# Kernel optimization log

Hardware: AMD Instinct MI355X
Metric: run time of the kernel (lower is better)

## Reference

```python
import jax, jax.numpy as jnp
import numpy as np

EPS = 1e-5  # torch BatchNorm2d default eps

def _bn_train(x, g, b):
    # BatchNorm2d in training mode: batch statistics over (N, H, W), biased variance
    m = x.mean(axis=(0, 2, 3), keepdims=True)
    v = x.var(axis=(0, 2, 3), keepdims=True)
    return g[None, :, None, None] * (x - m) / jnp.sqrt(v + EPS) + b[None, :, None, None]

def _conv3(x, w, b):
    y = jax.lax.conv_general_dilated(x, w, (1, 1), 'SAME',
                                     dimension_numbers=('NCHW', 'OIHW', 'NCHW'))
    return y + b[None, :, None, None]

def _conv1(x, w, b):
    # 1x1 conv == per-pixel matmul; w: [out, in]
    return jnp.einsum('bchw,oc->bohw', x, w) + b[None, :, None, None]

def _projector(x, w1, b1, g1, be1, w2, b2, g2, be2):
    h = jax.nn.relu(_bn_train(_conv3(x, w1, b1), g1, be1))
    return _bn_train(_conv1(h, w2, b2), g2, be2)

def _cross_teacher_attention(s, teachers, wq, bq, wk, bk, wv, bv):
    B, C, H, W = s.shape
    scale = C ** -0.5
    q = _conv1(s, wq, bq).reshape(B, C, H * W).transpose(0, 2, 1)  # [B, HW, C]
    outs, ws = [], []
    for t in teachers:  # small fixed list of teachers (structural branch)
        k = _conv1(t, wk, bk).reshape(B, C, H * W).transpose(0, 2, 1)
        v = _conv1(t, wv, bv).reshape(B, C, H * W).transpose(0, 2, 1)
        a = jax.nn.softmax(jnp.einsum('bqc,bkc->bqk', q, k) * scale, axis=-1)  # [B, HW, HW]
        outs.append(jnp.einsum('bqk,bkc->bqc', a, v))                          # [B, HW, C]
        ws.append(a.mean(axis=-1))                                             # [B, HW]
    w = jax.nn.softmax(jnp.stack(ws, axis=-1), axis=-1)          # [B, HW, T]
    fused = jnp.einsum('bqt,tbqc->bqc', w, jnp.stack(outs, 0))   # weighted sum over teachers
    fused = fused.reshape(B, H, W, C).transpose(0, 3, 1, 2)      # [B, C, H, W]
    return s + fused

def setup_inputs() -> dict:
    key = jax.random.key(0)
    ks = jax.random.split(key, 16)
    B, C, H, W = 8, 128, 56, 56
    T = 256  # teacher projector output dim
    d = {}
    d['student_mid'] = jax.random.normal(ks[0], (B, C, H, W), jnp.float32)
    d['t1_mid'] = jax.random.normal(ks[1], (B, C, H, W), jnp.float32)
    d['t2_mid'] = jax.random.normal(ks[2], (B, C, H, W), jnp.float32)
    for i, n in enumerate(['q', 'k', 'v']):
        d['w' + n] = jax.random.normal(ks[3 + i], (C, C), jnp.float32) * 0.05
        d['b' + n] = jnp.zeros((C,), jnp.float32)
    for p, off in (('p1', 6), ('p2', 10)):
        d[p + '_w1'] = jax.random.normal(ks[off], (C, C, 3, 3), jnp.float32) * 0.05
        d[p + '_b1'] = jnp.zeros((C,), jnp.float32)
        d[p + '_g1'] = jnp.ones((C,), jnp.float32)
        d[p + '_be1'] = jnp.zeros((C,), jnp.float32)
        d[p + '_w2'] = jax.random.normal(ks[off + 1], (T, C), jnp.float32) * 0.05
        d[p + '_b2'] = jnp.zeros((T,), jnp.float32)
        d[p + '_g2'] = jnp.ones((T,), jnp.float32)
        d[p + '_be2'] = jnp.zeros((T,), jnp.float32)
    return d

def reference(student_mid, t1_mid, t2_mid, wq, bq, wk, bk, wv, bv,
              p1_w1, p1_b1, p1_g1, p1_be1, p1_w2, p1_b2, p1_g2, p1_be2,
              p2_w1, p2_b1, p2_g1, p2_be1, p2_w2, p2_b2, p2_g2, p2_be2):
    # Per-teacher projectors: computed by the torch module but their outputs are
    # never consumed by the attention (s_feat_proj is unused) -> dead code.
    _sp1 = _projector(student_mid, p1_w1, p1_b1, p1_g1, p1_be1, p1_w2, p1_b2, p1_g2, p1_be2)
    _sp2 = _projector(student_mid, p2_w1, p2_b1, p2_g1, p2_be1, p2_w2, p2_b2, p2_g2, p2_be2)
    del _sp1, _sp2
    return _cross_teacher_attention(student_mid, [t1_mid, t2_mid], wq, bq, wk, bk, wv, bv)
```

## Files before the change

kernel.cpp:

```cpp
#include <hip/hip_runtime.h>

#define HW 3136
#define NB 8
#define CD 128
#define QSCALE 0.12751750206f

typedef __attribute__((ext_vector_type(8))) short short8;
typedef __attribute__((ext_vector_type(4))) float floatx4;
typedef __attribute__((ext_vector_type(4))) unsigned short ushort4v;

static __device__ __forceinline__ unsigned short f2b(float f){
  union { float f; unsigned u; } v; v.f = f;
  unsigned r = v.u + 0x7FFFu + ((v.u >> 16) & 1u);
  return (unsigned short)(r >> 16);
}
static __device__ __forceinline__ float b2f(unsigned short h){
  union { unsigned u; float f; } v; v.u = ((unsigned)h) << 16;
  return v.f;
}

__global__ __launch_bounds__(256) void proj_kernel(
    const float* __restrict__ s, const float* __restrict__ t1, const float* __restrict__ t2,
    const float* __restrict__ wq, const float* __restrict__ bq,
    const float* __restrict__ wk, const float* __restrict__ bk,
    const float* __restrict__ wv, const float* __restrict__ bv,
    unsigned short* __restrict__ qkv)
{
  __shared__ __align__(16) unsigned short WL[CD][136];
  __shared__ __align__(16) unsigned short xsT[64][136];
  const int job = blockIdx.z;
  const float* x; const float* w; const float* bias; float scl; int cmajor; size_t dstoff;
  switch(job){
    case 0: x=s;  w=wq; bias=bq; scl=QSCALE; cmajor=0; dstoff=0; break;
    case 1: x=t1; w=wk; bias=bk; scl=1.f;    cmajor=0; dstoff=1; break;
    case 2: x=t1; w=wv; bias=bv; scl=1.f;    cmajor=1; dstoff=2; break;
    case 3: x=t2; w=wk; bias=bk; scl=1.f;    cmajor=0; dstoff=3; break;
    default:x=t2; w=wv; bias=bv; scl=1.f;    cmajor=1; dstoff=4; break;
  }
  const size_t TS = (size_t)NB*HW*CD;
  const int b   = blockIdx.y;
  const int hw0 = blockIdx.x * 64;
  const int tid = threadIdx.x;

  for (int i = 0; i < 16; i++){
    int flat = tid + i*256;
    int o = flat >> 5, cq = (flat & 31)*4;
    floatx4 wv4 = *(const floatx4*)(w + (size_t)o*CD + cq);
    ushort4v pk;
    for (int j=0;j<4;j++) pk[j] = f2b(wv4[j]);
    *(ushort4v*)&WL[o][cq] = pk;
  }
  const float* xb = x + (size_t)b*CD*HW + hw0;
  for (int i = 0; i < 8; i++){
    int flat = (tid + i*256)*4;
    int c = flat >> 6, hh = flat & 63;
    floatx4 xv = *(const floatx4*)(xb + (size_t)c*HW + hh);
    for (int j=0;j<4;j++) xsT[hh+j][c] = f2b(xv[j]);
  }
  __syncthreads();

  const int m = tid & 15, quad = (tid >> 4) & 3, wv_ = tid >> 6;
  short8 af[4];
  for (int dk=0;dk<4;dk++)
    af[dk] = *(const short8*)&xsT[wv_*16 + m][dk*32 + quad*8];
  float bb[8];
  for (int nt=0;nt<8;nt++) bb[nt] = bias[nt*16 + m];

  unsigned short* dstK = qkv + dstoff*TS + ((size_t)b*HW + hw0)*CD;
  unsigned short* dstV = qkv + dstoff*TS + (size_t)b*CD*HW;
  for (int nt=0;nt<8;nt++){
    floatx4 acc = {bb[nt],bb[nt],bb[nt],bb[nt]};
    for (int dk=0;dk<4;dk++){
      short8 bf = *(const short8*)&WL[nt*16 + m][dk*32 + quad*8];
      acc = __builtin_amdgcn_mfma_f32_16x16x32_bf16(af[dk], bf, acc, 0,0,0);
    }
    if (!cmajor){
      for (int r=0;r<4;r++)
        dstK[(size_t)(wv_*16 + quad*4 + r)*CD + nt*16 + m] = f2b(acc[r]*scl);
    } else {
      ushort4v pk;
      for (int r=0;r<4;r++) pk[r] = f2b(acc[r]*scl);
      *(ushort4v*)&dstV[(size_t)(nt*16 + m)*HW + hw0 + wv_*16 + quad*4] = pk;
    }
  }
}

#define KL_E (64*136)
#define VL_E (128*72)
#define PL_E (4*16*72)

__global__ __launch_bounds__(256,3) void attn_kernel(
    const unsigned short* __restrict__ qkv,
    unsigned short* __restrict__ Og)
{
  __shared__ __align__(16) unsigned short smem[KL_E + VL_E + PL_E];
  unsigned short (*Kl)[136] = (unsigned short(*)[136])smem;
  unsigned short (*Vl)[72]  = (unsigned short(*)[72])(smem + KL_E);
  unsigned short (*Pl)[72]  = (unsigned short(*)[72])(smem + KL_E + VL_E);

  const int qt = blockIdx.x;
  const int b  = blockIdx.y;
  const int t  = blockIdx.z;
  const size_t TS = (size_t)NB*HW*CD;
  const unsigned short* Q = qkv + (size_t)b*HW*CD;
  const unsigned short* K = qkv + TS*(size_t)(1 + 2*t) + (size_t)b*HW*CD;
  const unsigned short* V = qkv + TS*(size_t)(2 + 2*t) + (size_t)b*CD*HW;

  const int tid  = threadIdx.x;
  const int wv_  = tid >> 6;
  const int lane = tid & 63;
  const int m    = lane & 15;
  const int quad = lane >> 4;
  const int q0   = qt*64 + wv_*16;

  short8 qf[4];
  {
    const unsigned short* qr = Q + (size_t)(q0+m)*CD + quad*8;
    for (int dk=0;dk<4;dk++) qf[dk] = *(const short8*)(qr + dk*32);
  }
  floatx4 Oc[8];
  for (int i=0;i<8;i++) Oc[i] = (floatx4)0.f;
  float lr[4] = {0.f,0.f,0.f,0.f};

  const unsigned short* kg = K + (size_t)(tid>>4)*CD + (tid&15)*8;
  const unsigned short* vg = V + (size_t)(tid>>3)*HW + (tid&7)*8;
  unsigned short* klds = &Kl[tid>>4][(tid&15)*8];
  unsigned short* vlds = &Vl[tid>>3][(tid&7)*8];

  short8 kpre[4], vpre[4];
  for (int i=0;i<4;i++) kpre[i] = *(const short8*)(kg + (size_t)i*16*CD);
  for (int i=0;i<4;i++) vpre[i] = *(const short8*)(vg + (size_t)i*32*HW);

  for (int kt = 0; kt < HW/64; kt++){
    __syncthreads();
    for (int i=0;i<4;i++) *(short8*)(klds + i*16*136) = kpre[i];
    for (int i=0;i<4;i++) *(short8*)(vlds + i*32*72)  = vpre[i];
    __syncthreads();
    if (kt < HW/64 - 1){
      kg += 64*CD; vg += 64;
      for (int i=0;i<4;i++) kpre[i] = *(const short8*)(kg + (size_t)i*16*CD);
      for (int i=0;i<4;i++) vpre[i] = *(const short8*)(vg + (size_t)i*32*HW);
    }

    floatx4 sc[4];
    for (int nt=0;nt<4;nt++){
      floatx4 acc = (floatx4)0.f;
      for (int dk=0;dk<4;dk++){
        short8 kf = *(const short8*)&Kl[nt*16 + m][dk*32 + quad*8];
        acc = __builtin_amdgcn_mfma_f32_16x16x32_bf16(qf[dk], kf, acc, 0,0,0);
      }
      sc[nt] = acc;
    }
    for (int nt=0;nt<4;nt++){
      for (int r=0;r<4;r++){
        float p = __builtin_amdgcn_exp2f(sc[nt][r]);
        lr[r] += p;
        union { float f; unsigned u; } cv; cv.f = p;
        Pl[wv_*16 + quad*4 + r][nt*16 + m] = (unsigned short)(cv.u >> 16);
      }
    }
    __asm__ volatile("s_waitcnt lgkmcnt(0)" ::: "memory");
    for (int ct=0;ct<8;ct++){
      floatx4 o = Oc[ct];
      for (int kk=0;kk<2;kk++){
        short8 pf = *(const short8*)&Pl[wv_*16 + m][kk*32 + quad*8];
        short8 vf = *(const short8*)&Vl[ct*16 + m][kk*32 + quad*8];
        o = __builtin_amdgcn_mfma_f32_16x16x32_bf16(pf, vf, o, 0,0,0);
      }
      Oc[ct] = o;
    }
  }

  for (int r=0;r<4;r++)
    for (int off=1; off<16; off<<=1)
      lr[r] += __shfl_xor(lr[r], off, 64);
  float inv[4];
  for (int r=0;r<4;r++) inv[r] = 1.f / lr[r];

  __syncthreads();
  float* stg = ((float*)smem) + wv_*(16*132);
  for (int ct=0;ct<8;ct++)
    for (int r=0;r<4;r++)
      stg[(quad*4+r)*132 + ct*16 + m] = Oc[ct][r]*inv[r];
  __syncthreads();
  unsigned short* ob = Og + ((size_t)t*NB + b)*HW*CD + (size_t)q0*CD;
  for (int row=0; row<16; row++){
    float v0 = stg[row*132 + 2*lane];
    float v1 = stg[row*132 + 2*lane + 1];
    unsigned short pk[2] = {f2b(v0), f2b(v1)};
    *(unsigned int*)&ob[(size_t)row*CD + 2*lane] = *(const unsigned int*)pk;
  }
}

__global__ __launch_bounds__(256) void combine_kernel(
    const float* __restrict__ s, const unsigned short* __restrict__ Og,
    float* __restrict__ out)
{
  __shared__ float T[32][129];
  const int b   = blockIdx.y;
  const int hw0 = blockIdx.x * 32;
  const int tid = threadIdx.x;
  const unsigned short* O1 = Og + ((size_t)b*HW + hw0)*CD;
  const unsigned short* O2 = O1 + (size_t)NB*HW*CD;
  for (int i=0;i<2;i++){
    int flat = (tid + i*256)*8;
    int row = flat >> 7, col = flat & 127;
    short8 a  = *(const short8*)(O1 + (size_t)row*CD + col);
    short8 c2 = *(const short8*)(O2 + (size_t)row*CD + col);
    for (int j=0;j<8;j++)
      T[row][col+j] = 0.5f*(b2f((unsigned short)a[j]) + b2f((unsigned short)c2[j]));
  }
  __syncthreads();
  const int c  = tid >> 1;
  const int h0 = (tid & 1)*16;
  const float* sr = s   + ((size_t)b*CD + c)*HW + hw0 + h0;
  float*     orow = out + ((size_t)b*CD + c)*HW + hw0 + h0;
  for (int j0=0;j0<16;j0+=4){
    floatx4 sv = *(const floatx4*)(sr + j0);
    floatx4 ov;
    for (int jj=0;jj<4;jj++) ov[jj] = sv[jj] + T[h0+j0+jj][c];
    *(floatx4*)(orow + j0) = ov;
  }
}

extern "C" void kernel_launch(void* const* d_in, const int* in_sizes, int n_in,
                              void* d_out, int out_size, void* d_ws, size_t ws_size,
                              hipStream_t stream)
{
  const float* s  = (const float*)d_in[0];
  const float* t1 = (const float*)d_in[1];
  const float* t2 = (const float*)d_in[2];
  const float* wq = (const float*)d_in[3];
  const float* bq = (const float*)d_in[4];
  const float* wk = (const float*)d_in[5];
  const float* bk = (const float*)d_in[6];
  const float* wv = (const float*)d_in[7];
  const float* bv = (const float*)d_in[8];
  float* out = (float*)d_out;

  unsigned short* qkv = (unsigned short*)d_ws;
  unsigned short* Og  = qkv + (size_t)5*NB*HW*CD;

  hipLaunchKernelGGL(proj_kernel,    dim3(49,8,5), dim3(256), 0, stream,
                     s,t1,t2,wq,bq,wk,bk,wv,bv,qkv);
  hipLaunchKernelGGL(attn_kernel,    dim3(49,8,2), dim3(256), 0, stream, qkv, Og);
  hipLaunchKernelGGL(combine_kernel, dim3(98,8),   dim3(256), 0, stream, s, Og, out);
}
```

Before: 310.1 us.

## Use 32x32 MFMA with register-resident P in attention and batch-loop projection

The attention kernel moves to 32x32x16 bf16 MFMA with 128-query tiles per block. It computes S transposed so the exponentiated scores stay in registers and are swapped between half-waves with a shuffle, instead of passing through an LDS P buffer. LDS strides and occupancy bounds also change, and the final normalization and store are restaged. The projection kernel now loops over the batch inside each block, double-buffering the transposed input and reusing the loaded weight tile, which cuts the grid from 1960 to 245 blocks. The risks are lower occupancy and parallelism in proj, padded last query tiles, and possible bank conflicts from the new LDS strides.

Result: slower. 568.2 us (+83.2%).

```diff
diff --git a/kernel.cpp b/kernel.cpp
--- a/kernel.cpp
+++ b/kernel.cpp
@@ -7,6 +7,7 @@
 
 typedef __attribute__((ext_vector_type(8))) short short8;
 typedef __attribute__((ext_vector_type(4))) float floatx4;
+typedef __attribute__((ext_vector_type(16))) float floatx16;
 typedef __attribute__((ext_vector_type(4))) unsigned short ushort4v;
 
 static __device__ __forceinline__ unsigned short f2b(float f){
@@ -14,12 +15,16 @@
   unsigned r = v.u + 0x7FFFu + ((v.u >> 16) & 1u);
   return (unsigned short)(r >> 16);
 }
+static __device__ __forceinline__ unsigned short f2b_trunc(float f){
+  union { float f; unsigned u; } v; v.f = f;
+  return (unsigned short)(v.u >> 16);
+}
 static __device__ __forceinline__ float b2f(unsigned short h){
   union { unsigned u; float f; } v; v.u = ((unsigned)h) << 16;
   return v.f;
 }
 
-__global__ __launch_bounds__(256) void proj_kernel(
+__global__ __launch_bounds__(256,2) void proj_kernel(
     const float* __restrict__ s, const float* __restrict__ t1, const float* __restrict__ t2,
     const float* __restrict__ wq, const float* __restrict__ bq,
     const float* __restrict__ wk, const float* __restrict__ bk,
@@ -27,8 +32,8 @@
     unsigned short* __restrict__ qkv)
 {
   __shared__ __align__(16) unsigned short WL[CD][136];
-  __shared__ __align__(16) unsigned short xsT[64][136];
-  const int job = blockIdx.z;
+  __shared__ __align__(16) unsigned short XT[2][64][136];
+  const int job = blockIdx.y;
   const float* x; const float* w; const float* bias; float scl; int cmajor; size_t dstoff;
   switch(job){
     case 0: x=s;  w=wq; bias=bq; scl=QSCALE; cmajor=0; dstoff=0; break;
@@ -38,7 +43,6 @@
     default:x=t2; w=wv; bias=bv; scl=1.f;    cmajor=1; dstoff=4; break;
   }
   const size_t TS = (size_t)NB*HW*CD;
-  const int b   = blockIdx.y;
   const int hw0 = blockIdx.x * 64;
   const int tid = threadIdx.x;
 
@@ -50,53 +54,71 @@
     for (int j=0;j<4;j++) pk[j] = f2b(wv4[j]);
     *(ushort4v*)&WL[o][cq] = pk;
   }
-  const float* xb = x + (size_t)b*CD*HW + hw0;
-  for (int i = 0; i < 8; i++){
-    int flat = (tid + i*256)*4;
-    int c = flat >> 6, hh = flat & 63;
-    floatx4 xv = *(const floatx4*)(xb + (size_t)c*HW + hh);
-    for (int j=0;j<4;j++) xsT[hh+j][c] = f2b(xv[j]);
-  }
-  __syncthreads();
 
   const int m = tid & 15, quad = (tid >> 4) & 3, wv_ = tid >> 6;
-  short8 af[4];
-  for (int dk=0;dk<4;dk++)
-    af[dk] = *(const short8*)&xsT[wv_*16 + m][dk*32 + quad*8];
   float bb[8];
   for (int nt=0;nt<8;nt++) bb[nt] = bias[nt*16 + m];
 
-  unsigned short* dstK = qkv + dstoff*TS + ((size_t)b*HW + hw0)*CD;
-  unsigned short* dstV = qkv + dstoff*TS + (size_t)b*CD*HW;
-  for (int nt=0;nt<8;nt++){
-    floatx4 acc = {bb[nt],bb[nt],bb[nt],bb[nt]};
-    for (int dk=0;dk<4;dk++){
-      short8 bf = *(const short8*)&WL[nt*16 + m][dk*32 + quad*8];
-      acc = __builtin_amdgcn_mfma_f32_16x16x32_bf16(af[dk], bf, acc, 0,0,0);
-    }
-    if (!cmajor){
-      for (int r=0;r<4;r++)
-        dstK[(size_t)(wv_*16 + quad*4 + r)*CD + nt*16 + m] = f2b(acc[r]*scl);
-    } else {
-      ushort4v pk;
-      for (int r=0;r<4;r++) pk[r] = f2b(acc[r]*scl);
-      *(ushort4v*)&dstV[(size_t)(nt*16 + m)*HW + hw0 + wv_*16 + quad*4] = pk;
-    }
-  }
-}
-
-#define KL_E (64*136)
-#define VL_E (128*72)
-#define PL_E (4*16*72)
-
-__global__ __launch_bounds__(256,3) void attn_kernel(
+  {
+    const float* xb = x + hw0;
+    for (int i = 0; i < 8; i++){
+      int flat = (tid + i*256)*4;
+      int c = flat >> 6, hh = flat & 63;
+      floatx4 xv = *(const floatx4*)(xb + (size_t)c*HW + hh);
+      for (int j=0;j<4;j++) XT[0][hh+j][c] = f2b(xv[j]);
+    }
+  }
+
+  for (int b = 0; b < NB; b++){
+    __syncthreads();
+    if (b+1 < NB){
+      const float* xb = x + (size_t)(b+1)*CD*HW + hw0;
+      int buf = (b+1)&1;
+      for (int i = 0; i < 8; i++){
+        int flat = (tid + i*256)*4;
+        int c = flat >> 6, hh = flat & 63;
+        floatx4 xv = *(const floatx4*)(xb + (size_t)c*HW + hh);
+        for (int j=0;j<4;j++) XT[buf][hh+j][c] = f2b(xv[j]);
+      }
+    }
+    const int cur = b & 1;
+    short8 af[4];
+    for (int dk=0;dk<4;dk++)
+      af[dk] = *(const short8*)&XT[cur][wv_*16 + m][dk*32 + quad*8];
+
+    unsigned short* dstK = qkv + dstoff*TS + ((size_t)b*HW + hw0)*CD;
+    unsigned short* dstV = qkv + dstoff*TS + (size_t)b*CD*HW;
+    for (int nt=0;nt<8;nt++){
+      floatx4 acc = {bb[nt],bb[nt],bb[nt],bb[nt]};
+      for (int dk=0;dk<4;dk++){
+        short8 bf = *(const short8*)&WL[nt*16 + m][dk*32 + quad*8];
+        acc = __builtin_amdgcn_mfma_f32_16x16x32_bf16(af[dk], bf, acc, 0,0,0);
+      }
+      if (!cmajor){
+        for (int r=0;r<4;r++)
+          dstK[(size_t)(wv_*16 + quad*4 + r)*CD + nt*16 + m] = f2b(acc[r]*scl);
+      } else {
+        ushort4v pk;
+        for (int r=0;r<4;r++) pk[r] = f2b(acc[r]*scl);
+        *(ushort4v*)&dstV[(size_t)(nt*16 + m)*HW + hw0 + wv_*16 + quad*4] = pk;
+      }
+    }
+  }
+}
+
+#define KSTR 132
+#define VSTR 68
+#define KL_E (64*KSTR)
+#define VL_E (128*VSTR)
+
+__global__ __launch_bounds__(256,2) void attn_kernel(
     const unsigned short* __restrict__ qkv,
     unsigned short* __restrict__ Og)
 {
-  __shared__ __align__(16) unsigned short smem[KL_E + VL_E + PL_E];
-  unsigned short (*Kl)[136] = (unsigned short(*)[136])smem;
-  unsigned short (*Vl)[72]  = (unsigned short(*)[72])(smem + KL_E);
-  unsigned short (*Pl)[72]  = (unsigned short(*)[72])(smem + KL_E + VL_E);
+  __shared__ __align__(16) unsigned short smem[KL_E + VL_E];
+  __shared__ float invL[4][32];
+  unsigned short (*Kl)[KSTR] = (unsigned short(*)[KSTR])smem;
+  unsigned short (*Vl)[VSTR] = (unsigned short(*)[VSTR])(smem + KL_E);
 
   const int qt = blockIdx.x;
   const int b  = blockIdx.y;
@@ -107,20 +129,21 @@
   const unsigned short* V = qkv + TS*(size_t)(2 + 2*t) + (size_t)b*CD*HW;
 
   const int tid  = threadIdx.x;
-  const int wv_  = tid >> 6;
+  const int w    = tid >> 6;
   const int lane = tid & 63;
-  const int m    = lane & 15;
-  const int quad = lane >> 4;
-  const int q0   = qt*64 + wv_*16;
-
-  short8 qf[4];
+  const int ln   = lane & 31;
+  const int h    = lane >> 5;
+  const int q0w  = qt*128 + w*32;
+
+  short8 qf[8];
   {
-    const unsigned short* qr = Q + (size_t)(q0+m)*CD + quad*8;
-    for (int dk=0;dk<4;dk++) qf[dk] = *(const short8*)(qr + dk*32);
-  }
-  floatx4 Oc[8];
-  for (int i=0;i<8;i++) Oc[i] = (floatx4)0.f;
-  float lr[4] = {0.f,0.f,0.f,0.f};
+    int qrow = q0w + ln; if (qrow >= HW) qrow = HW-1;
+    const unsigned short* qr = Q + (size_t)qrow*CD + h*8;
+    for (int dk=0;dk<8;dk++) qf[dk] = *(const short8*)(qr + dk*16);
+  }
+  floatx16 Oc[4];
+  for (int i=0;i<4;i++) Oc[i] = (floatx16)0.f;
+  float lr = 0.f;
 
   const unsigned short* kg = K + (size_t)(tid>>4)*CD + (tid&15)*8;
   const unsigned short* vg = V + (size_t)(tid>>3)*HW + (tid&7)*8;
@@ -133,8 +156,8 @@
 
   for (int kt = 0; kt < HW/64; kt++){
     __syncthreads();
-    for (int i=0;i<4;i++) *(short8*)(klds + i*16*136) = kpre[i];
-    for (int i=0;i<4;i++) *(short8*)(vlds + i*32*72)  = vpre[i];
+    for (int i=0;i<4;i++) *(short8*)(klds + i*16*KSTR) = kpre[i];
+    for (int i=0;i<4;i++) *(short8*)(vlds + i*32*VSTR) = vpre[i];
     __syncthreads();
     if (kt < HW/64 - 1){
       kg += 64*CD; vg += 64;
@@ -142,53 +165,64 @@
       for (int i=0;i<4;i++) vpre[i] = *(const short8*)(vg + (size_t)i*32*HW);
     }
 
-    floatx4 sc[4];
-    for (int nt=0;nt<4;nt++){
-      floatx4 acc = (floatx4)0.f;
-      for (int dk=0;dk<4;dk++){
-        short8 kf = *(const short8*)&Kl[nt*16 + m][dk*32 + quad*8];
-        acc = __builtin_amdgcn_mfma_f32_16x16x32_bf16(qf[dk], kf, acc, 0,0,0);
-      }
-      sc[nt] = acc;
-    }
-    for (int nt=0;nt<4;nt++){
-      for (int r=0;r<4;r++){
-        float p = __builtin_amdgcn_exp2f(sc[nt][r]);
-        lr[r] += p;
-        union { float f; unsigned u; } cv; cv.f = p;
-        Pl[wv_*16 + quad*4 + r][nt*16 + m] = (unsigned short)(cv.u >> 16);
-      }
-    }
-    __asm__ volatile("s_waitcnt lgkmcnt(0)" ::: "memory");
-    for (int ct=0;ct<8;ct++){
-      floatx4 o = Oc[ct];
-      for (int kk=0;kk<2;kk++){
-        short8 pf = *(const short8*)&Pl[wv_*16 + m][kk*32 + quad*8];
-        short8 vf = *(const short8*)&Vl[ct*16 + m][kk*32 + quad*8];
-        o = __builtin_amdgcn_mfma_f32_16x16x32_bf16(pf, vf, o, 0,0,0);
-      }
-      Oc[ct] = o;
-    }
-  }
-
-  for (int r=0;r<4;r++)
-    for (int off=1; off<16; off<<=1)
-      lr[r] += __shfl_xor(lr[r], off, 64);
-  float inv[4];
-  for (int r=0;r<4;r++) inv[r] = 1.f / lr[r];
-
+    floatx16 s0 = (floatx16)0.f, s1 = (floatx16)0.f;
+    for (int dk=0;dk<8;dk++){
+      short8 kf = *(const short8*)&Kl[ln][dk*16 + h*8];
+      s0 = __builtin_amdgcn_mfma_f32_32x32x16_bf16(kf, qf[dk], s0, 0,0,0);
+    }
+    for (int dk=0;dk<8;dk++){
+      short8 kf = *(const short8*)&Kl[32 + ln][dk*16 + h*8];
+      s1 = __builtin_amdgcn_mfma_f32_32x32x16_bf16(kf, qf[dk], s1, 0,0,0);
+    }
+    for (int r=0;r<16;r++){ s0[r] = __builtin_amdgcn_exp2f(s0[r]); lr += s0[r]; }
+    for (int r=0;r<16;r++){ s1[r] = __builtin_amdgcn_exp2f(s1[r]); lr += s1[r]; }
+
+#define PV_STEP(SV, KS)                                                        \
+    {                                                                          \
+      short8 pf;                                                               \
+      _Pragma("unroll")                                                        \
+      for (int b2=0;b2<4;b2++){                                                \
+        const int r0 = ((KS)&1)*8 + b2, r1 = r0 + 4;                           \
+        float own = h ? (SV)[r1] : (SV)[r0];                                   \
+        float snd = h ? (SV)[r0] : (SV)[r1];                                   \
+        float oth = __shfl_xor(snd, 32, 64);                                   \
+        float fl  = h ? oth : own;                                             \
+        float fh  = h ? own : oth;                                             \
+        pf[b2]   = (short)f2b_trunc(fl);                                       \
+        pf[4+b2] = (short)f2b_trunc(fh);                                       \
+      }                                                                        \
+      _Pragma("unroll")                                                        \
+      for (int ct=0;ct<4;ct++){                                                \
+        short8 vf = *(const short8*)&Vl[ct*32 + ln][(KS)*16 + h*8];            \
+        Oc[ct] = __builtin_amdgcn_mfma_f32_32x32x16_bf16(pf, vf, Oc[ct], 0,0,0);\
+      }                                                                        \
+    }
+    PV_STEP(s0, 0) PV_STEP(s0, 1) PV_STEP(s1, 2) PV_STEP(s1, 3)
+#undef PV_STEP
+  }
+
+  lr += __shfl_xor(lr, 32, 64);
+  float inv = 1.f / lr;
   __syncthreads();
-  float* stg = ((float*)smem) + wv_*(16*132);
-  for (int ct=0;ct<8;ct++)
-    for (int r=0;r<4;r++)
-      stg[(quad*4+r)*132 + ct*16 + m] = Oc[ct][r]*inv[r];
-  __syncthreads();
-  unsigned short* ob = Og + ((size_t)t*NB + b)*HW*CD + (size_t)q0*CD;
-  for (int row=0; row<16; row++){
-    float v0 = stg[row*132 + 2*lane];
-    float v1 = stg[row*132 + 2*lane + 1];
-    unsigned short pk[2] = {f2b(v0), f2b(v1)};
-    *(unsigned int*)&ob[(size_t)row*CD + 2*lane] = *(const unsigned int*)pk;
+  if (h == 0) invL[w][ln] = inv;
+  __asm__ volatile("s_waitcnt lgkmcnt(0)" ::: "memory");
+  float iv[16];
+  for (int r=0;r<16;r++) iv[r] = invL[w][(r&3) + 8*(r>>2) + 4*h];
+
+  unsigned short* stg = smem + w*(32*KSTR);
+  for (int ct=0;ct<4;ct++)
+    for (int r=0;r<16;r++){
+      int row = (r&3) + 8*(r>>2) + 4*h;
+      stg[row*KSTR + ct*32 + ln] = f2b(Oc[ct][r]*iv[r]);
+    }
+  __asm__ volatile("s_waitcnt lgkmcnt(0)" ::: "memory");
+  if (q0w < HW){
+    unsigned short* ob = Og + ((size_t)t*NB + b)*HW*CD + (size_t)q0w*CD;
+    for (int i=0;i<16;i++){
+      int row2 = i*2 + h;
+      ushort4v v4 = *(const ushort4v*)&stg[row2*KSTR + ln*4];
+      *(ushort4v*)&ob[(size_t)row2*CD + ln*4] = v4;
+    }
   }
 }
 
@@ -241,8 +275,8 @@
   unsigned short* qkv = (unsigned short*)d_ws;
   unsigned short* Og  = qkv + (size_t)5*NB*HW*CD;
 
-  hipLaunchKernelGGL(proj_kernel,    dim3(49,8,5), dim3(256), 0, stream,
+  hipLaunchKernelGGL(proj_kernel,    dim3(49,5),   dim3(256), 0, stream,
                      s,t1,t2,wq,bq,wk,bk,wv,bv,qkv);
-  hipLaunchKernelGGL(attn_kernel,    dim3(49,8,2), dim3(256), 0, stream, qkv, Og);
+  hipLaunchKernelGGL(attn_kernel,    dim3(25,8,2), dim3(256), 0, stream, qkv, Og);
   hipLaunchKernelGGL(combine_kernel, dim3(98,8),   dim3(256), 0, stream, s, Og, out);
 }
```
